# Performance work log

Hardware: AMD Instinct MI355X
Metric: run time of the kernel (lower is better)

## Reference

```python
import jax, jax.numpy as jnp
import numpy as np

NUM_GRAPHS_N = 64  # number of segments in node_batch
NUM_GRAPHS_L = 64  # number of segments in label_batch


def setup_inputs() -> dict:
    key = jax.random.key(0)
    k1, k2, k3, k4, k5 = jax.random.split(key, 5)
    N, D = 16384, 256
    En, El = 8192, 8192
    h = jax.random.normal(k1, (N, D), dtype=jnp.float32)
    node_edge = jax.random.randint(k2, (2, En), 0, N, dtype=jnp.int64)
    node_batch = jnp.sort(jax.random.randint(k3, (En,), 0, NUM_GRAPHS_N, dtype=jnp.int64))
    label_edge = jax.random.randint(k4, (2, El), 0, N, dtype=jnp.int64)
    label_batch = jnp.sort(jax.random.randint(k5, (El,), 0, NUM_GRAPHS_L, dtype=jnp.int64))
    return {"h": h, "node_edge": node_edge, "node_batch": node_batch,
            "label_edge": label_edge, "label_batch": label_batch}


def _cdist(a, b):
    # Euclidean pairwise distance, grad-safe sqrt.
    sq = (jnp.sum(a * a, -1)[:, None] + jnp.sum(b * b, -1)[None, :]
          - 2.0 * (a @ b.T))
    sq = jnp.maximum(sq, 0.0)
    safe = jnp.where(sq > 0, sq, 1.0)
    return jnp.where(sq > 0, jnp.sqrt(safe), 0.0)


def _seg_max(x, seg, num):  # max over axis 0; empty segments -> 0 like torch_scatter
    m = jax.ops.segment_max(x, seg, num_segments=num)
    return jnp.where(jnp.isfinite(m), m, 0.0)


def _seg_mean(x, seg, num):
    s = jax.ops.segment_sum(x, seg, num_segments=num)
    cnt = jax.ops.segment_sum(jnp.ones((x.shape[0], 1), x.dtype), seg, num_segments=num)
    return s / jnp.maximum(cnt, 1.0)


def reference(h, node_edge, node_batch, label_edge, label_batch):
    ef_n = (h[node_edge[0]] + h[node_edge[1]]) * 0.5   # [En, D]
    ef_l = (h[label_edge[0]] + h[label_edge[1]]) * 0.5  # [El, D]
    M = -_cdist(ef_n, ef_l)                              # [En, El]
    # max over cols by label_batch -> [En, Gl], then mean over rows by node_batch
    out_n = _seg_max(M.T, label_batch, NUM_GRAPHS_L).T   # [En, Gl]
    out_n = _seg_mean(out_n, node_batch, NUM_GRAPHS_N)   # [Gn, Gl]
    # max over rows by node_batch -> [Gn, El], then mean over cols by label_batch
    out_l = _seg_max(M, node_batch, NUM_GRAPHS_N)        # [Gn, El]
    out_l = _seg_mean(out_l.T, label_batch, NUM_GRAPHS_L).T  # [Gn, Gl]
    return (out_n + out_l) * 0.5
```

## Files before the change

### kernel.cpp

```cpp
#include <hip/hip_runtime.h>
#include <hip/hip_bf16.h>
#include <math.h>

#define EN 8192
#define EL 8192
#define D  256
#define NG 64
#define INF_BITS 0x7f800000u

typedef __attribute__((ext_vector_type(8))) short  bf16x8;
typedef __attribute__((ext_vector_type(4))) float  f32x4;

__device__ __forceinline__ unsigned short f2bf(float f) {
    unsigned u = __float_as_uint(f);
    unsigned r = (u + 0x7fffu + ((u >> 16) & 1u)) >> 16;
    return (unsigned short)r;
}

__device__ __forceinline__ float dpp_min16(float m) {
    float t;
    asm("v_min_f32 %0, %1, %2 quad_perm:[1,0,3,2] row_mask:0xf bank_mask:0xf"
        : "=v"(t) : "v"(m), "v"(m));
    asm("v_min_f32 %0, %1, %2 quad_perm:[2,3,0,1] row_mask:0xf bank_mask:0xf"
        : "=v"(m) : "v"(t), "v"(t));
    asm("v_min_f32 %0, %1, %2 row_ror:4 row_mask:0xf bank_mask:0xf"
        : "=v"(t) : "v"(m), "v"(m));
    asm("v_min_f32 %0, %1, %2 row_ror:8 row_mask:0xf bank_mask:0xf"
        : "=v"(m) : "v"(t), "v"(t));
    return m;
}

__device__ __forceinline__ float pl16_min(float m) {
    float a = m, b = m;
    asm volatile("v_permlane16_swap_b32 %0, %1" : "+v"(a), "+v"(b));
    return fminf(a, b);
}
__device__ __forceinline__ float pl32_min(float m) {
    float a = m, b = m;
    asm volatile("v_permlane32_swap_b32 %0, %1" : "+v"(a), "+v"(b));
    return fminf(a, b);
}
__device__ __forceinline__ float fmin3(float a, float b, float c) {
    float d;
    asm("v_min3_f32 %0, %1, %2, %3" : "=v"(d) : "v"(a), "v"(b), "v"(c));
    return d;
}

__global__ void prep(const float* __restrict__ h,
                     const int* __restrict__ node_edge,
                     const int* __restrict__ label_edge,
                     unsigned short* __restrict__ efn, float* __restrict__ normN,
                     unsigned short* __restrict__ efl, float* __restrict__ normL,
                     unsigned* __restrict__ inf_buf)
{
    int b = blockIdx.x;
    if (b < 1024) {
        uint4 v = make_uint4(INF_BITS, INF_BITS, INF_BITS, INF_BITS);
        ((uint4*)inf_buf)[b * 256 + threadIdx.x] = v;
        return;
    }
    b -= 1024;
    const int* edges; unsigned short* ef; float* norm;
    if (b < 2048) { edges = node_edge;  ef = efn; norm = normN; }
    else          { b -= 2048; edges = label_edge; ef = efl; norm = normL; }

    int wave = threadIdx.x >> 6;
    int lane = threadIdx.x & 63;
    int e = b * 4 + wave;
    int a  = edges[e];
    int bb = edges[EN + e];
    float4 va = ((const float4*)(h + (size_t)a  * D))[lane];
    float4 vb = ((const float4*)(h + (size_t)bb * D))[lane];
    float4 f;
    f.x = 0.5f * (va.x + vb.x);
    f.y = 0.5f * (va.y + vb.y);
    f.z = 0.5f * (va.z + vb.z);
    f.w = 0.5f * (va.w + vb.w);
    float sq = f.x*f.x + f.y*f.y + f.z*f.z + f.w*f.w;
    ushort4 pk;
    pk.x = f2bf(f.x); pk.y = f2bf(f.y); pk.z = f2bf(f.z); pk.w = f2bf(f.w);
    ((ushort4*)(ef + (size_t)e * D))[lane] = pk;
    #pragma unroll
    for (int off = 1; off < 64; off <<= 1)
        sq += __shfl_xor(sq, off, 64);
    if (lane == 0) norm[e] = sq;
}

#define BARRIER()  asm volatile("s_barrier" ::: "memory")
#define VMCNT4()   asm volatile("s_waitcnt vmcnt(4)" ::: "memory")
#define VMCNT0()   asm volatile("s_waitcnt vmcnt(0)" ::: "memory")

__launch_bounds__(512, 4)
__global__ void dist_min(const unsigned short* __restrict__ A,
                         const unsigned short* __restrict__ B,
                         const float* __restrict__ normN,
                         const float* __restrict__ normL,
                         const int* __restrict__ node_batch,
                         const int* __restrict__ label_batch,
                         unsigned* __restrict__ bufN,
                         unsigned* __restrict__ bufL)
{
    __shared__ unsigned short As[2][128 * 64];
    __shared__ unsigned short Bs[2][128 * 64];

    const int tid  = threadIdx.x;
    const int lane = tid & 63;
    const int wave = tid >> 6;
    const int quad = lane >> 4;
    const int lc   = lane & 15;

    const int lin    = blockIdx.y * 64 + blockIdx.x;
    const int xcd    = lin & 7;
    const int within = lin >> 3;
    const int tx     = within & 15;
    const int ty     = within >> 4;
    const int m0 = ((xcd >> 2) * 32 + ty) * 128;
    const int n0 = ((xcd & 3) * 16 + tx) * 128;

    const int wr   = (wave >> 1) * 32;
    const int wc   = (wave & 1) * 64;

    float nb[4]; int gl[4];
    #pragma unroll
    for (int ni = 0; ni < 4; ++ni) {
        int col = n0 + wc + ni*16 + lc;
        nb[ni] = normL[col];
        gl[ni] = label_batch[col];
    }
    float na[8]; int gr[8];
    #pragma unroll
    for (int mi = 0; mi < 2; ++mi)
        #pragma unroll
        for (int r = 0; r < 4; ++r) {
            int row = m0 + wr + mi*16 + quad*4 + r;
            na[mi*4 + r] = normN[row];
            gr[mi*4 + r] = node_batch[row];
        }
    const int glo = label_batch[n0 + wc], ghi = label_batch[n0 + wc + 63];
    const int rlo = node_batch[m0 + wr], rhi = node_batch[m0 + wr + 31];

    f32x4 acc[2][4];
    #pragma unroll
    for (int i = 0; i < 2; ++i)
        #pragma unroll
        for (int j = 0; j < 4; ++j) {
            f32x4 z = {0.f, 0.f, 0.f, 0.f};
            acc[i][j] = z;
        }

    auto stage = [&](int buf, int kt) {
        #pragma unroll
        for (int t = 0; t < 2; ++t) {
            int c = t * 512 + tid;
            int row = c >> 3, cc = c & 7;
            int scc = cc ^ (row & 7);
            const unsigned short* gp = A + (size_t)(m0 + row) * D + kt * 64 + scc * 8;
            __builtin_amdgcn_global_load_lds(
                (const __attribute__((address_space(1))) void*)gp,
                (__attribute__((address_space(3))) void*)(As[buf] + c * 8), 16, 0, 0);
        }
        #pragma unroll
        for (int t = 0; t < 2; ++t) {
            int c = t * 512 + tid;
            int row = c >> 3, cc = c & 7;
            int scc = cc ^ (row & 7);
            const unsigned short* gp = B + (size_t)(n0 + row) * D + kt * 64 + scc * 8;
            __builtin_amdgcn_global_load_lds(
                (const __attribute__((address_space(1))) void*)gp,
                (__attribute__((address_space(3))) void*)(Bs[buf] + c * 8), 16, 0, 0);
        }
    };

    auto compute = [&](const unsigned short* Asb, const unsigned short* Bsb) {
        #pragma unroll
        for (int kk = 0; kk < 2; ++kk) {
            bf16x8 af[2], bfv[4];
            #pragma unroll
            for (int mi = 0; mi < 2; ++mi)
                af[mi] = *(const bf16x8*)(Asb + (wr + mi*16 + lc) * 64
                                             + ((kk*4 + quad) ^ (lc & 7)) * 8);
            #pragma unroll
            for (int ni = 0; ni < 4; ++ni)
                bfv[ni] = *(const bf16x8*)(Bsb + (wc + ni*16 + lc) * 64
                                              + ((kk*4 + quad) ^ (lc & 7)) * 8);
            __builtin_amdgcn_s_setprio(1);
            #pragma unroll
            for (int mi = 0; mi < 2; ++mi)
                #pragma unroll
                for (int ni = 0; ni < 4; ++ni)
                    acc[mi][ni] = __builtin_amdgcn_mfma_f32_16x16x32_bf16(
                        af[mi], bfv[ni], acc[mi][ni], 0, 0, 0);
            __builtin_amdgcn_s_setprio(0);
        }
    };

    stage(0, 0);
    stage(1, 1);
    VMCNT4();
    BARRIER();

    compute(As[0], Bs[0]);
    BARRIER();
    stage(0, 2);
    VMCNT4();
    BARRIER();

    compute(As[1], Bs[1]);
    BARRIER();
    stage(1, 3);
    VMCNT4();
    BARRIER();

    compute(As[0], Bs[0]);
    VMCNT0();
    BARRIER();

    compute(As[1], Bs[1]);

    #pragma unroll
    for (int mi = 0; mi < 2; ++mi)
        #pragma unroll
        for (int ni = 0; ni < 4; ++ni)
            #pragma unroll
            for (int r = 0; r < 4; ++r)
                acc[mi][ni][r] = fmaxf(
                    fmaf(-2.0f, acc[mi][ni][r], na[mi*4 + r] + nb[ni]), 0.0f);

    const float FINF = __uint_as_float(INF_BITS);

    if (glo == ghi) {
        float rm[8];
        #pragma unroll
        for (int mi = 0; mi < 2; ++mi)
            #pragma unroll
            for (int r = 0; r < 4; ++r) {
                float m = fminf(fmin3(acc[mi][0][r], acc[mi][1][r], acc[mi][2][r]),
                                acc[mi][3][r]);
                rm[mi*4 + r] = dpp_min16(m);
            }
        if (lc == 0) {
            #pragma unroll
            for (int mi = 0; mi < 2; ++mi)
                #pragma unroll
                for (int r = 0; r < 4; ++r) {
                    int row = m0 + wr + mi*16 + quad*4 + r;
                    atomicMin(&bufN[row * NG + glo], __float_as_uint(rm[mi*4 + r]));
                }
        }
    } else {
        for (int g = glo; g <= ghi; ++g) {
            bool s0 = (gl[0] == g), s1 = (gl[1] == g), s2 = (gl[2] == g), s3 = (gl[3] == g);
            float rm[8];
            #pragma unroll
            for (int mi = 0; mi < 2; ++mi)
                #pragma unroll
                for (int r = 0; r < 4; ++r) {
                    float v0 = s0 ? acc[mi][0][r] : FINF;
                    float v1 = s1 ? acc[mi][1][r] : FINF;
                    float v2 = s2 ? acc[mi][2][r] : FINF;
                    float v3 = s3 ? acc[mi][3][r] : FINF;
                    rm[mi*4 + r] = dpp_min16(fminf(fmin3(v0, v1, v2), v3));
                }
            if (lc == 0) {
                #pragma unroll
                for (int mi = 0; mi < 2; ++mi)
                    #pragma unroll
                    for (int r = 0; r < 4; ++r) {
                        int row = m0 + wr + mi*16 + quad*4 + r;
                        atomicMin(&bufN[row * NG + g], __float_as_uint(rm[mi*4 + r]));
                    }
            }
        }
    }

    if (rlo == rhi) {
        float cm[4];
        #pragma unroll
        for (int ni = 0; ni < 4; ++ni) {
            float m = fminf(fmin3(fmin3(acc[0][ni][0], acc[0][ni][1], acc[0][ni][2]),
                                  fmin3(acc[0][ni][3], acc[1][ni][0], acc[1][ni][1]),
                                  acc[1][ni][2]),
                            acc[1][ni][3]);
            m = pl16_min(m);
            m = pl32_min(m);
            cm[ni] = m;
        }
        if (quad == 0) {
            #pragma unroll
            for (int ni = 0; ni < 4; ++ni) {
                int col = n0 + wc + ni*16 + lc;
                atomicMin(&bufL[rlo * EL + col], __float_as_uint(cm[ni]));
            }
        }
    } else {
        for (int g = rlo; g <= rhi; ++g) {
            float cm[4];
            #pragma unroll
            for (int ni = 0; ni < 4; ++ni) {
                float s[8];
                #pragma unroll
                for (int mi = 0; mi < 2; ++mi)
                    #pragma unroll
                    for (int r = 0; r < 4; ++r)
                        s[mi*4 + r] = (gr[mi*4 + r] == g) ? acc[mi][ni][r] : FINF;
                float m = fminf(fmin3(fmin3(s[0], s[1], s[2]),
                                      fmin3(s[3], s[4], s[5]), s[6]),
                                s[7]);
                m = pl16_min(m);
                m = pl32_min(m);
                cm[ni] = m;
            }
            if (quad == 0) {
                #pragma unroll
                for (int ni = 0; ni < 4; ++ni) {
                    int col = n0 + wc + ni*16 + lc;
                    atomicMin(&bufL[g * EL + col], __float_as_uint(cm[ni]));
                }
            }
        }
    }
}

__device__ __forceinline__ int lbound(const int* __restrict__ a, int n, int v) {
    int lo = 0, hi = n;
    while (lo < hi) { int mid = (lo + hi) >> 1; if (a[mid] < v) lo = mid + 1; else hi = mid; }
    return lo;
}

__global__ void finalize(const unsigned* __restrict__ bufN,
                         const unsigned* __restrict__ bufL,
                         const int* __restrict__ node_batch,
                         const int* __restrict__ label_batch,
                         float* __restrict__ out)
{
    __shared__ float sN[NG];
    __shared__ float sL[NG];
    int gn  = blockIdx.x;
    int tid = threadIdx.x;
    if (tid < NG) { sN[tid] = 0.0f; sL[tid] = 0.0f; }
    __syncthreads();

    int ns = lbound(node_batch, EN, gn);
    int ne = lbound(node_batch, EN, gn + 1);

    {
        int t = tid & 63, strip = tid >> 6;
        float acc = 0.0f;
        for (int i = ns + strip; i < ne; i += 16) {
            unsigned b = bufN[i * NG + t];
            if (b != INF_BITS) acc -= sqrtf(__uint_as_float(b));
        }
        atomicAdd(&sN[t], acc);
    }

    for (int j = tid; j < EL; j += 1024) {
        unsigned b = bufL[gn * EL + j];
        if (b != INF_BITS) {
            int g = label_batch[j];
            atomicAdd(&sL[g], -sqrtf(__uint_as_float(b)));
        }
    }
    __syncthreads();

    if (tid < NG) {
        int t = tid;
        int cn = ne - ns;
        int ls = lbound(label_batch, EL, t);
        int le = lbound(label_batch, EL, t + 1);
        int cl = le - ls;
        float out_n = sN[t] / (float)(cn > 0 ? cn : 1);
        float out_l = sL[t] / (float)(cl > 0 ? cl : 1);
        out[gn * NG + t] = 0.5f * (out_n + out_l);
    }
}

extern "C" void kernel_launch(void* const* d_in, const int* in_sizes, int n_in,
                              void* d_out, int out_size, void* d_ws, size_t ws_size,
                              hipStream_t stream)
{
    const float* h          = (const float*)d_in[0];
    const int* node_edge    = (const int*)d_in[1];
    const int* node_batch   = (const int*)d_in[2];
    const int* label_edge   = (const int*)d_in[3];
    const int* label_batch  = (const int*)d_in[4];
    float* out = (float*)d_out;

    char* ws = (char*)d_ws;
    unsigned short* efn = (unsigned short*)ws; ws += (size_t)EN * D * 2;
    unsigned short* efl = (unsigned short*)ws; ws += (size_t)EL * D * 2;
    float* normN = (float*)ws;                 ws += (size_t)EN * 4;
    float* normL = (float*)ws;                 ws += (size_t)EL * 4;
    unsigned* bufN = (unsigned*)ws;            ws += (size_t)EN * NG * 4;
    unsigned* bufL = (unsigned*)ws;            ws += (size_t)NG * EL * 4;

    prep<<<5120, 256, 0, stream>>>(h, node_edge, label_edge,
                                   efn, normN, efl, normL, bufN);
    dist_min<<<dim3(EL / 128, EN / 128), 512, 0, stream>>>(
        efn, efl, normN, normL, node_batch, label_batch, bufN, bufL);
    finalize<<<NG, 1024, 0, stream>>>(bufN, bufL, node_batch, label_batch, out);
}
```

Baseline: 178.2 us.

## Process two column tiles per block, overlapping first epilogue with next loads

```diff
diff --git a/kernel.cpp b/kernel.cpp
--- a/kernel.cpp
+++ b/kernel.cpp
@@ -109,24 +109,18 @@
     const int quad = lane >> 4;
     const int lc   = lane & 15;
 
-    const int lin    = blockIdx.y * 64 + blockIdx.x;
+    const int lin    = blockIdx.y * 32 + blockIdx.x;
     const int xcd    = lin & 7;
     const int within = lin >> 3;
-    const int tx     = within & 15;
-    const int ty     = within >> 4;
-    const int m0 = ((xcd >> 2) * 32 + ty) * 128;
-    const int n0 = ((xcd & 3) * 16 + tx) * 128;
+    const int txp    = within & 7;
+    const int ty     = within >> 3;
+    const int m0  = ((xcd >> 2) * 32 + ty) * 128;
+    const int n0a = ((xcd & 3) * 16 + txp * 2) * 128;
+    const int n0b = n0a + 128;
 
     const int wr   = (wave >> 1) * 32;
     const int wc   = (wave & 1) * 64;
 
-    float nb[4]; int gl[4];
-    #pragma unroll
-    for (int ni = 0; ni < 4; ++ni) {
-        int col = n0 + wc + ni*16 + lc;
-        nb[ni] = normL[col];
-        gl[ni] = label_batch[col];
-    }
     float na[8]; int gr[8];
     #pragma unroll
     for (int mi = 0; mi < 2; ++mi)
@@ -136,19 +130,32 @@
             na[mi*4 + r] = normN[row];
             gr[mi*4 + r] = node_batch[row];
         }
-    const int glo = label_batch[n0 + wc], ghi = label_batch[n0 + wc + 63];
     const int rlo = node_batch[m0 + wr], rhi = node_batch[m0 + wr + 31];
 
+    float nbA[4], nbB[4]; int glA[4], glB[4];
+    #pragma unroll
+    for (int ni = 0; ni < 4; ++ni) {
+        int colA = n0a + wc + ni*16 + lc;
+        int colB = n0b + wc + ni*16 + lc;
+        nbA[ni] = normL[colA];  glA[ni] = label_batch[colA];
+        nbB[ni] = normL[colB];  glB[ni] = label_batch[colB];
+    }
+    const int gloA = label_batch[n0a + wc], ghiA = label_batch[n0a + wc + 63];
+    const int gloB = label_batch[n0b + wc], ghiB = label_batch[n0b + wc + 63];
+
     f32x4 acc[2][4];
-    #pragma unroll
-    for (int i = 0; i < 2; ++i)
-        #pragma unroll
-        for (int j = 0; j < 4; ++j) {
-            f32x4 z = {0.f, 0.f, 0.f, 0.f};
-            acc[i][j] = z;
-        }
-
-    auto stage = [&](int buf, int kt) {
+    auto zero_acc = [&]() {
+        #pragma unroll
+        for (int i = 0; i < 2; ++i)
+            #pragma unroll
+            for (int j = 0; j < 4; ++j) {
+                f32x4 z = {0.f, 0.f, 0.f, 0.f};
+                acc[i][j] = z;
+            }
+    };
+    zero_acc();
+
+    auto stage = [&](int buf, int n0t, int kt) {
         #pragma unroll
         for (int t = 0; t < 2; ++t) {
             int c = t * 512 + tid;
@@ -164,7 +171,7 @@
             int c = t * 512 + tid;
             int row = c >> 3, cc = c & 7;
             int scc = cc ^ (row & 7);
-            const unsigned short* gp = B + (size_t)(n0 + row) * D + kt * 64 + scc * 8;
+            const unsigned short* gp = B + (size_t)(n0t + row) * D + kt * 64 + scc * 8;
             __builtin_amdgcn_global_load_lds(
                 (const __attribute__((address_space(1))) void*)gp,
                 (__attribute__((address_space(3))) void*)(Bs[buf] + c * 8), 16, 0, 0);
@@ -194,72 +201,28 @@
         }
     };
 
-    stage(0, 0);
-    stage(1, 1);
-    VMCNT4();
-    BARRIER();
-
-    compute(As[0], Bs[0]);
-    BARRIER();
-    stage(0, 2);
-    VMCNT4();
-    BARRIER();
-
-    compute(As[1], Bs[1]);
-    BARRIER();
-    stage(1, 3);
-    VMCNT4();
-    BARRIER();
-
-    compute(As[0], Bs[0]);
-    VMCNT0();
-    BARRIER();
-
-    compute(As[1], Bs[1]);
-
-    #pragma unroll
-    for (int mi = 0; mi < 2; ++mi)
-        #pragma unroll
-        for (int ni = 0; ni < 4; ++ni)
-            #pragma unroll
-            for (int r = 0; r < 4; ++r)
-                acc[mi][ni][r] = fmaxf(
-                    fmaf(-2.0f, acc[mi][ni][r], na[mi*4 + r] + nb[ni]), 0.0f);
-
     const float FINF = __uint_as_float(INF_BITS);
 
-    if (glo == ghi) {
-        float rm[8];
+    auto do_epilogue = [&](int n0t, const float* nb, const int* gl,
+                           int glo, int ghi) {
         #pragma unroll
         for (int mi = 0; mi < 2; ++mi)
             #pragma unroll
-            for (int r = 0; r < 4; ++r) {
-                float m = fminf(fmin3(acc[mi][0][r], acc[mi][1][r], acc[mi][2][r]),
-                                acc[mi][3][r]);
-                rm[mi*4 + r] = dpp_min16(m);
-            }
-        if (lc == 0) {
+            for (int ni = 0; ni < 4; ++ni)
+                #pragma unroll
+                for (int r = 0; r < 4; ++r)
+                    acc[mi][ni][r] = fmaxf(
+                        fmaf(-2.0f, acc[mi][ni][r], na[mi*4 + r] + nb[ni]), 0.0f);
+
+        if (glo == ghi) {
+            float rm[8];
             #pragma unroll
             for (int mi = 0; mi < 2; ++mi)
                 #pragma unroll
                 for (int r = 0; r < 4; ++r) {
-                    int row = m0 + wr + mi*16 + quad*4 + r;
-                    atomicMin(&bufN[row * NG + glo], __float_as_uint(rm[mi*4 + r]));
-                }
-        }
-    } else {
-        for (int g = glo; g <= ghi; ++g) {
-            bool s0 = (gl[0] == g), s1 = (gl[1] == g), s2 = (gl[2] == g), s3 = (gl[3] == g);
-            float rm[8];
-            #pragma unroll
-            for (int mi = 0; mi < 2; ++mi)
-                #pragma unroll
-                for (int r = 0; r < 4; ++r) {
-                    float v0 = s0 ? acc[mi][0][r] : FINF;
-                    float v1 = s1 ? acc[mi][1][r] : FINF;
-                    float v2 = s2 ? acc[mi][2][r] : FINF;
-                    float v3 = s3 ? acc[mi][3][r] : FINF;
-                    rm[mi*4 + r] = dpp_min16(fminf(fmin3(v0, v1, v2), v3));
+                    float m = fminf(fmin3(acc[mi][0][r], acc[mi][1][r], acc[mi][2][r]),
+                                    acc[mi][3][r]);
+                    rm[mi*4 + r] = dpp_min16(m);
                 }
             if (lc == 0) {
                 #pragma unroll
@@ -267,45 +230,44 @@
                     #pragma unroll
                     for (int r = 0; r < 4; ++r) {
                         int row = m0 + wr + mi*16 + quad*4 + r;
-                        atomicMin(&bufN[row * NG + g], __float_as_uint(rm[mi*4 + r]));
+                        atomicMin(&bufN[row * NG + glo], __float_as_uint(rm[mi*4 + r]));
                     }
             }
-        }
-    }
-
-    if (rlo == rhi) {
-        float cm[4];
-        #pragma unroll
-        for (int ni = 0; ni < 4; ++ni) {
-            float m = fminf(fmin3(fmin3(acc[0][ni][0], acc[0][ni][1], acc[0][ni][2]),
-                                  fmin3(acc[0][ni][3], acc[1][ni][0], acc[1][ni][1]),
-                                  acc[1][ni][2]),
-                            acc[1][ni][3]);
-            m = pl16_min(m);
-            m = pl32_min(m);
-            cm[ni] = m;
-        }
-        if (quad == 0) {
-            #pragma unroll
-            for (int ni = 0; ni < 4; ++ni) {
-                int col = n0 + wc + ni*16 + lc;
-                atomicMin(&bufL[rlo * EL + col], __float_as_uint(cm[ni]));
-            }
-        }
-    } else {
-        for (int g = rlo; g <= rhi; ++g) {
-            float cm[4];
-            #pragma unroll
-            for (int ni = 0; ni < 4; ++ni) {
-                float s[8];
+        } else {
+            for (int g = glo; g <= ghi; ++g) {
+                bool s0 = (gl[0] == g), s1 = (gl[1] == g),
+                     s2 = (gl[2] == g), s3 = (gl[3] == g);
+                float rm[8];
                 #pragma unroll
                 for (int mi = 0; mi < 2; ++mi)
                     #pragma unroll
-                    for (int r = 0; r < 4; ++r)
-                        s[mi*4 + r] = (gr[mi*4 + r] == g) ? acc[mi][ni][r] : FINF;
-                float m = fminf(fmin3(fmin3(s[0], s[1], s[2]),
-                                      fmin3(s[3], s[4], s[5]), s[6]),
-                                s[7]);
+                    for (int r = 0; r < 4; ++r) {
+                        float v0 = s0 ? acc[mi][0][r] : FINF;
+                        float v1 = s1 ? acc[mi][1][r] : FINF;
+                        float v2 = s2 ? acc[mi][2][r] : FINF;
+                        float v3 = s3 ? acc[mi][3][r] : FINF;
+                        rm[mi*4 + r] = dpp_min16(fminf(fmin3(v0, v1, v2), v3));
+                    }
+                if (lc == 0) {
+                    #pragma unroll
+                    for (int mi = 0; mi < 2; ++mi)
+                        #pragma unroll
+                        for (int r = 0; r < 4; ++r) {
+                            int row = m0 + wr + mi*16 + quad*4 + r;
+                            atomicMin(&bufN[row * NG + g], __float_as_uint(rm[mi*4 + r]));
+                        }
+                }
+            }
+        }
+
+        if (rlo == rhi) {
+            float cm[4];
+            #pragma unroll
+            for (int ni = 0; ni < 4; ++ni) {
+                float m = fminf(fmin3(fmin3(acc[0][ni][0], acc[0][ni][1], acc[0][ni][2]),
+                                      fmin3(acc[0][ni][3], acc[1][ni][0], acc[1][ni][1]),
+                                      acc[1][ni][2]),
+                                acc[1][ni][3]);
                 m = pl16_min(m);
                 m = pl32_min(m);
                 cm[ni] = m;
@@ -313,12 +275,89 @@
             if (quad == 0) {
                 #pragma unroll
                 for (int ni = 0; ni < 4; ++ni) {
-                    int col = n0 + wc + ni*16 + lc;
-                    atomicMin(&bufL[g * EL + col], __float_as_uint(cm[ni]));
+                    int col = n0t + wc + ni*16 + lc;
+                    atomicMin(&bufL[rlo * EL + col], __float_as_uint(cm[ni]));
                 }
             }
-        }
-    }
+        } else {
+            for (int g = rlo; g <= rhi; ++g) {
+                float cm[4];
+                #pragma unroll
+                for (int ni = 0; ni < 4; ++ni) {
+                    float s[8];
+                    #pragma unroll
+                    for (int mi = 0; mi < 2; ++mi)
+                        #pragma unroll
+                        for (int r = 0; r < 4; ++r)
+                            s[mi*4 + r] = (gr[mi*4 + r] == g) ? acc[mi][ni][r] : FINF;
+                    float m = fminf(fmin3(fmin3(s[0], s[1], s[2]),
+                                          fmin3(s[3], s[4], s[5]), s[6]),
+                                    s[7]);
+                    m = pl16_min(m);
+                    m = pl32_min(m);
+                    cm[ni] = m;
+                }
+                if (quad == 0) {
+                    #pragma unroll
+                    for (int ni = 0; ni < 4; ++ni) {
+                        int col = n0t + wc + ni*16 + lc;
+                        atomicMin(&bufL[g * EL + col], __float_as_uint(cm[ni]));
+                    }
+                }
+            }
+        }
+    };
+
+    stage(0, n0a, 0);
+    stage(1, n0a, 1);
+    VMCNT4();
+    BARRIER();
+
+    compute(As[0], Bs[0]);
+    BARRIER();
+    stage(0, n0a, 2);
+    VMCNT4();
+    BARRIER();
+
+    compute(As[1], Bs[1]);
+    BARRIER();
+    stage(1, n0a, 3);
+    VMCNT4();
+    BARRIER();
+
+    compute(As[0], Bs[0]);
+    BARRIER();
+    stage(0, n0b, 0);
+    VMCNT4();
+    BARRIER();
+
+    compute(As[1], Bs[1]);
+    BARRIER();
+    stage(1, n0b, 1);
+    VMCNT4();
+    do_epilogue(n0a, nbA, glA, gloA, ghiA);
+    zero_acc();
+    BARRIER();
+
+    compute(As[0], Bs[0]);
+    BARRIER();
+    stage(0, n0b, 2);
+    VMCNT4();
+    BARRIER();
+
+    compute(As[1], Bs[1]);
+    BARRIER();
+    stage(1, n0b, 3);
+    VMCNT4();
+    BARRIER();
+
+    compute(As[0], Bs[0]);
+    VMCNT0();
+    BARRIER();
+
+    compute(As[1], Bs[1]);
+
+    do_epilogue(n0b, nbB, glB, gloB, ghiB);
 }
 
 __device__ __forceinline__ int lbound(const int* __restrict__ a, int n, int v) {
@@ -395,7 +434,7 @@
 
     prep<<<5120, 256, 0, stream>>>(h, node_edge, label_edge,
                                    efn, normN, efl, normL, bufN);
-    dist_min<<<dim3(EL / 128, EN / 128), 512, 0, stream>>>(
+    dist_min<<<dim3(32, 64), 512, 0, stream>>>(
         efn, efl, normN, normL, node_batch, label_batch, bufN, bufL);
     finalize<<<NG, 1024, 0, stream>>>(bufN, bufL, node_batch, label_batch, out);
 }
```

Result: no change. 178.1 us (-0.1%).
